# Performance work log

Hardware: AMD Instinct MI355X
Metric: run time of the kernel (lower is better)

The kernel has to match this reference:

```python
import jax, jax.numpy as jnp
import numpy as np

D_MODEL = 1024
N_HEADS = 16
HEAD_DIM = D_MODEL // N_HEADS


def setup_inputs() -> dict:
    key = jax.random.key(0)
    ks = jax.random.split(key, 9)
    B, S = 2, 2048
    s = 1.0 / np.sqrt(D_MODEL)
    return {
        "x": jax.random.normal(ks[0], (B, S, D_MODEL), dtype=jnp.float32),
        "Wq": jax.random.normal(ks[1], (D_MODEL, D_MODEL), dtype=jnp.float32) * s,
        "bq": jnp.zeros((D_MODEL,), dtype=jnp.float32),
        "Wk": jax.random.normal(ks[2], (D_MODEL, D_MODEL), dtype=jnp.float32) * s,
        "bk": jnp.zeros((D_MODEL,), dtype=jnp.float32),
        "Wv": jax.random.normal(ks[3], (D_MODEL, D_MODEL), dtype=jnp.float32) * s,
        "bv": jnp.zeros((D_MODEL,), dtype=jnp.float32),
        "Wo": jax.random.normal(ks[4], (D_MODEL, D_MODEL), dtype=jnp.float32) * s,
        "bo": jnp.zeros((D_MODEL,), dtype=jnp.float32),
    }


def reference(x, Wq, bq, Wk, bk, Wv, bv, Wo, bo):
    B, S, D = x.shape
    H, Hd = N_HEADS, HEAD_DIM
    # projections; torch Linear: x @ W^T + b -> here W stored as [in, out]
    q = (x @ Wq + bq).reshape(B, S, H, Hd).transpose(0, 2, 1, 3)  # [B,H,S,Hd]
    k = (x @ Wk + bk).reshape(B, S, H, Hd).transpose(0, 2, 1, 3)
    v = (x @ Wv + bv).reshape(B, S, H, Hd).transpose(0, 2, 1, 3)
    scores = jnp.einsum("bhsd,bhtd->bhst", q, k) / jnp.sqrt(jnp.float32(Hd))
    causal = jnp.tril(jnp.ones((S, S), dtype=bool))  # True = keep
    scores = jnp.where(causal, scores, jnp.float32(-jnp.inf))
    attn = jax.nn.softmax(scores, axis=-1)
    out = jnp.einsum("bhst,bhtd->bhsd", attn, v)  # [B,H,S,Hd]
    out = out.transpose(0, 2, 1, 3).reshape(B, S, D)
    return out @ Wo + bo
```

## Files before the change

### kernel.cpp

```cpp
#include <hip/hip_runtime.h>
#include <hip/hip_bf16.h>
#include <cmath>

#define D_MODEL 1024
#define N_HEADS 16
#define HEAD_DIM 64
#define SEQ 2048
#define BATCH 2
#define MROWS (BATCH * SEQ)

typedef __bf16 bf16;
typedef __bf16 bf16x8 __attribute__((ext_vector_type(8)));
typedef __bf16 bf16x4 __attribute__((ext_vector_type(4)));
typedef float f32x4 __attribute__((ext_vector_type(4)));

#define SWZG(row, cbyte) ((row) * 64 + ((cbyte) ^ ((((row) >> 1) & 3) << 4)))

#define GLOAD16(g, l)                                                        \
    __builtin_amdgcn_global_load_lds(                                        \
        (const __attribute__((address_space(1))) void*)(g),                  \
        (__attribute__((address_space(3))) void*)(l), 16, 0, 0)

static __device__ __forceinline__ unsigned short bfbits(float f) {
    bf16 b = (bf16)f;
    return *(unsigned short*)&b;
}

__global__ __launch_bounds__(256) void cvt_x(const float* __restrict__ x,
                                             bf16* __restrict__ xb) {
    int i = blockIdx.x * 256 + threadIdx.x;
    float4 v = ((const float4*)x)[i];
    bf16x4 o = { (bf16)v.x, (bf16)v.y, (bf16)v.z, (bf16)v.w };
    ((bf16x4*)xb)[i] = o;
}

__global__ void cvt_wt(const float* __restrict__ Wq, const float* __restrict__ Wk,
                       const float* __restrict__ Wv, const float* __restrict__ Wo,
                       bf16* __restrict__ wt) {
    __shared__ float tile[32][33];
    int z = blockIdx.z;
    const float* W = (z == 0) ? Wq : (z == 1) ? Wk : (z == 2) ? Wv : Wo;
    int n0 = blockIdx.x * 32, k0 = blockIdx.y * 32;
    int tx = threadIdx.x, ty = threadIdx.y;
    tile[ty][tx] = W[(size_t)(k0 + ty) * D_MODEL + n0 + tx];
    __syncthreads();
    wt[(size_t)z * D_MODEL * D_MODEL + (size_t)(n0 + ty) * D_MODEL + k0 + tx] =
        (bf16)tile[tx][ty];
}

template <int MODE>
__global__ __launch_bounds__(256) void gemm_k(const bf16* __restrict__ A,
                                              const bf16* __restrict__ Bt,
                                              const float* __restrict__ b0,
                                              const float* __restrict__ b1,
                                              const float* __restrict__ b2,
                                              void* __restrict__ outp) {
    constexpr int BM = 128, BK = 32, KDIM = D_MODEL;
    __shared__ alignas(16) char SMEM[49152];
    char* Asb = SMEM;
    char* Bsb = SMEM + 24576;
    const int tid = threadIdx.x;
    const int wid = tid >> 6, lane = tid & 63;
    const int m0 = blockIdx.y * BM, n0 = blockIdx.x * BM;
    const int wr = (wid >> 1) * 64, wc = (wid & 1) * 64;
    f32x4 acc[4][4] = {};

#define GSTAGE(K0, BUF)                                                       \
    {                                                                         \
        _Pragma("unroll") for (int c = 0; c < 2; ++c) {                       \
            const int q = c * 4 + wid;                                        \
            const int row = q * 16 + (lane >> 2);                             \
            const int col = (lane & 3) ^ ((row >> 1) & 3);                    \
            GLOAD16(&A[(size_t)(m0 + row) * KDIM + (K0) + col * 8],           \
                    Asb + (BUF) * 8192 + q * 1024);                           \
            GLOAD16(&Bt[(size_t)(n0 + row) * KDIM + (K0) + col * 8],          \
                    Bsb + (BUF) * 8192 + q * 1024);                           \
        }                                                                     \
    }

    GSTAGE(0, 0);
    GSTAGE(BK, 1);
    int cur = 0;
    for (int k0 = 0; k0 < KDIM; k0 += BK) {
        if (k0 + 2 * BK < KDIM) {
            int nb = cur + 2;
            if (nb >= 3) nb -= 3;
            GSTAGE(k0 + 2 * BK, nb);
            asm volatile("s_waitcnt vmcnt(8)" ::: "memory");
        } else if (k0 + BK < KDIM) {
            asm volatile("s_waitcnt vmcnt(4)" ::: "memory");
        } else {
            asm volatile("s_waitcnt vmcnt(0)" ::: "memory");
        }
        __builtin_amdgcn_s_barrier();

        char* Ab = Asb + cur * 8192;
        char* Bb = Bsb + cur * 8192;
        const int cb = (lane >> 4) * 16;
        bf16x8 a[4], b[4];
#pragma unroll
        for (int m = 0; m < 4; ++m) {
            int r = wr + m * 16 + (lane & 15);
            a[m] = *(bf16x8*)(Ab + SWZG(r, cb));
        }
#pragma unroll
        for (int n = 0; n < 4; ++n) {
            int r = wc + n * 16 + (lane & 15);
            b[n] = *(bf16x8*)(Bb + SWZG(r, cb));
        }
#pragma unroll
        for (int m = 0; m < 4; ++m)
#pragma unroll
            for (int n = 0; n < 4; ++n)
                acc[m][n] = __builtin_amdgcn_mfma_f32_16x16x32_bf16(a[m], b[n], acc[m][n], 0, 0, 0);

        __builtin_amdgcn_s_barrier();
        cur = (cur == 2) ? 0 : cur + 1;
    }
#undef GSTAGE

    const int z = n0 >> 10;
    const float* bias = (MODE == 1) ? b0 : ((z == 0) ? b0 : (z == 1) ? b1 : b2);

    if (MODE == 0 && z == 2) {
        bf16* T = (bf16*)SMEM;
#pragma unroll
        for (int m = 0; m < 4; ++m)
#pragma unroll
            for (int n = 0; n < 4; ++n)
#pragma unroll
                for (int r = 0; r < 4; ++r) {
                    int ml = wr + m * 16 + (lane >> 4) * 4 + r;
                    int nl = wc + n * 16 + (lane & 15);
                    float val = acc[m][n][r] + bias[(n0 & 1023) + nl];
                    *(bf16*)((char*)T + nl * 256 + ((2 * ml) ^ ((nl & 7) << 4))) = (bf16)val;
                }
        __builtin_amdgcn_s_barrier();
        const int b_ = m0 >> 11;
        const int s_base = m0 & 2047;
#pragma unroll
        for (int c = 0; c < 8; ++c) {
            int idx = c * 256 + tid;
            int nl = idx >> 4, j = idx & 15;
            bf16x8 v = *(bf16x8*)((char*)T + nl * 256 + ((16 * j) ^ ((nl & 7) << 4)));
            int colN = (n0 & 1023) + nl;
            int head = colN >> 6, hd = colN & 63;
            *(bf16x8*)&((bf16*)outp)[(size_t)2 * 4194304 +
                                     ((size_t)(b_ * N_HEADS + head) * HEAD_DIM + hd) * SEQ +
                                     s_base + 8 * j] = v;
        }
        return;
    }

#pragma unroll
    for (int m = 0; m < 4; ++m)
#pragma unroll
        for (int n = 0; n < 4; ++n)
#pragma unroll
            for (int r = 0; r < 4; ++r) {
                int grow = m0 + wr + m * 16 + (lane >> 4) * 4 + r;
                int gcol = n0 + wc + n * 16 + (lane & 15);
                if (MODE == 0) {
                    int colN = gcol & 1023;
                    float val = acc[m][n][r] + bias[colN];
                    if (z == 0) val *= 0.125f;
                    int b_ = grow >> 11, s_ = grow & 2047;
                    int h = colN >> 6, hd = colN & 63;
                    ((bf16*)outp)[(size_t)z * 4194304 +
                                  ((size_t)(b_ * N_HEADS + h) * SEQ + s_) * HEAD_DIM + hd] =
                        (bf16)val;
                } else {
                    float val = acc[m][n][r] + bias[gcol];
                    ((float*)outp)[(size_t)grow * D_MODEL + gcol] = val;
                }
            }
}

__global__ __launch_bounds__(512) void attn_k(const bf16* __restrict__ Qg,
                                              const bf16* __restrict__ Kg,
                                              const bf16* __restrict__ VTg,
                                              bf16* __restrict__ AO) {
    __shared__ alignas(16) bf16 Ks[2][64 * 64];
    __shared__ alignas(16) bf16 Vs[2][64 * 64];
    __shared__ alignas(16) unsigned int Pk[8][16][32];
    const int tid = threadIdx.x, wid = tid >> 6, lane = tid & 63;
    const int m = lane & 15, h = lane >> 4;
    const int band = 15 - (int)(blockIdx.x >> 5);
    const int bh = blockIdx.x & 31;
    const int q0 = band * 128 + wid * 16;
    const size_t base = (size_t)bh * SEQ * HEAD_DIM;
    const bf16* VT = VTg + (size_t)bh * HEAD_DIM * SEQ;
    const int swz = (m & 7) << 2;
    const int nt_w = band * 2 + (wid >> 2) + 1;
    const int nt_blk = band * 2 + 2;

    bf16x8 aq[2];
#pragma unroll
    for (int kc = 0; kc < 2; ++kc)
        aq[kc] = *(const bf16x8*)
            &Qg[base + (size_t)(q0 + m) * HEAD_DIM + kc * 32 + h * 8];

    f32x4 o[4] = {};
    float mrow = -__builtin_inff();
    float lrow = 0.f;

#define STAGE(T0, BUF)                                                            \
    {                                                                             \
        int row = tid >> 3, sl = tid & 7;                                         \
        GLOAD16(&Kg[base + (size_t)((T0) + row) * HEAD_DIM + 8 * (sl ^ (row & 7))], \
                (char*)&Ks[BUF][0] + tid * 16);                                   \
        GLOAD16(&VT[(size_t)row * SEQ + (T0) + 8 * (sl ^ (row & 7))],             \
                (char*)&Vs[BUF][0] + tid * 16);                                   \
    }

    STAGE(0, 0);
    int cur = 0;
    for (int it = 0; it < nt_blk; ++it) {
        if (it + 1 < nt_blk) {
            STAGE((it + 1) * 64, cur ^ 1);
            asm volatile("s_waitcnt vmcnt(2)" ::: "memory");
        } else {
            asm volatile("s_waitcnt vmcnt(0)" ::: "memory");
        }
        __builtin_amdgcn_s_barrier();

        if (it < nt_w) {
            const int t0 = it * 64;
            char* Kb = (char*)&Ks[cur][0];
            char* Vb = (char*)&Vs[cur][0];
            bf16x8 kf[4][2], vf[4][2];
#pragma unroll
            for (int tf = 0; tf < 4; ++tf)
#pragma unroll
                for (int kc = 0; kc < 2; ++kc)
                    kf[tf][kc] = *(bf16x8*)(Kb + (16 * tf + m) * 128 +
                                            (((4 * kc + h) ^ (m & 7)) << 4));
#pragma unroll
            for (int nf = 0; nf < 4; ++nf)
#pragma unroll
                for (int kc = 0; kc < 2; ++kc)
                    vf[nf][kc] = *(bf16x8*)(Vb + (16 * nf + m) * 128 +
                                            (((4 * kc + h) ^ (m & 7)) << 4));

            f32x4 s[4];
            __builtin_amdgcn_s_setprio(1);
#pragma unroll
            for (int tf = 0; tf < 4; ++tf) {
                f32x4 z = {};
                z = __builtin_amdgcn_mfma_f32_16x16x32_bf16(kf[tf][0], aq[0], z, 0, 0, 0);
                z = __builtin_amdgcn_mfma_f32_16x16x32_bf16(kf[tf][1], aq[1], z, 0, 0, 0);
                s[tf] = z;
            }
            __builtin_amdgcn_s_setprio(0);

            if (it == nt_w - 1) {
#pragma unroll
                for (int tf = 0; tf < 4; ++tf)
#pragma unroll
                    for (int r = 0; r < 4; ++r) {
                        int gq = q0 + m;
                        int gt = t0 + tf * 16 + h * 4 + r;
                        if (gt > gq) s[tf][r] = -__builtin_inff();
                    }
            }

            float mx = s[0][0];
#pragma unroll
            for (int tf = 0; tf < 4; ++tf)
#pragma unroll
                for (int r = 0; r < 4; ++r) mx = fmaxf(mx, s[tf][r]);
            mx = fmaxf(mx, __shfl_xor(mx, 16));
            mx = fmaxf(mx, __shfl_xor(mx, 32));
            if (!__all(mx <= mrow + 8.f)) {
                float mn = fmaxf(mrow, mx);
                float sf = __expf(mrow - mn);
                mrow = mn;
                lrow *= sf;
                float sfr[4];
#pragma unroll
                for (int r = 0; r < 4; ++r) sfr[r] = __shfl(sf, 20 * h + r);
#pragma unroll
                for (int nf = 0; nf < 4; ++nf)
#pragma unroll
                    for (int r = 0; r < 4; ++r) o[nf][r] *= sfr[r];
            }
            float rs = 0.f;
#pragma unroll
            for (int tf = 0; tf < 4; ++tf)
#pragma unroll
                for (int r = 0; r < 4; ++r) {
                    float pv = __expf(s[tf][r] - mrow);
                    s[tf][r] = pv;
                    rs += pv;
                }
            rs += __shfl_xor(rs, 16);
            rs += __shfl_xor(rs, 32);
            lrow += rs;

#pragma unroll
            for (int tf = 0; tf < 4; ++tf)
#pragma unroll
                for (int rp = 0; rp < 2; ++rp) {
                    unsigned int w = ((unsigned int)bfbits(s[tf][2 * rp + 1]) << 16) |
                                     bfbits(s[tf][2 * rp]);
                    Pk[wid][m][(8 * tf + 2 * h + rp) ^ swz] = w;
                }

            __builtin_amdgcn_s_setprio(1);
#pragma unroll
            for (int kc = 0; kc < 2; ++kc) {
                bf16x8 ap = *(bf16x8*)&Pk[wid][m][(16 * kc + 4 * h) ^ swz];
#pragma unroll
                for (int nf = 0; nf < 4; ++nf)
                    o[nf] = __builtin_amdgcn_mfma_f32_16x16x32_bf16(
                        ap, vf[nf][kc], o[nf], 0, 0, 0);
            }
            __builtin_amdgcn_s_setprio(0);
        }
        __builtin_amdgcn_s_barrier();
        cur ^= 1;
    }
#undef STAGE

    const int b_ = bh >> 4, hh = bh & 15;
    float lcr[4];
#pragma unroll
    for (int r = 0; r < 4; ++r) lcr[r] = __shfl(lrow, 20 * h + r);
#pragma unroll
    for (int nf = 0; nf < 4; ++nf)
#pragma unroll
        for (int r = 0; r < 4; ++r) {
            float val = o[nf][r] / lcr[r];
            int s_ = q0 + h * 4 + r;
            AO[((size_t)(b_ * SEQ + s_)) * D_MODEL + hh * HEAD_DIM + nf * 16 + m] =
                (bf16)val;
        }
}

extern "C" void kernel_launch(void* const* d_in, const int* in_sizes, int n_in,
                              void* d_out, int out_size, void* d_ws, size_t ws_size,
                              hipStream_t stream) {
    const float* x  = (const float*)d_in[0];
    const float* Wq = (const float*)d_in[1];
    const float* bq = (const float*)d_in[2];
    const float* Wk = (const float*)d_in[3];
    const float* bk = (const float*)d_in[4];
    const float* Wv = (const float*)d_in[5];
    const float* bv = (const float*)d_in[6];
    const float* Wo = (const float*)d_in[7];
    const float* bo = (const float*)d_in[8];

    char* ws = (char*)d_ws;
    const size_t MB = 1u << 20;
    bf16* wt = (bf16*)ws;
    bf16* xb = (bf16*)(ws + 8 * MB);
    bf16* Qb = (bf16*)(ws + 16 * MB);
    bf16* AO = (bf16*)(ws + 40 * MB);

    const size_t WSTRIDE = (size_t)D_MODEL * D_MODEL;

    cvt_x<<<dim3(MROWS * D_MODEL / 4 / 256), dim3(256), 0, stream>>>(x, xb);
    cvt_wt<<<dim3(32, 32, 4), dim3(32, 32), 0, stream>>>(Wq, Wk, Wv, Wo, wt);

    gemm_k<0><<<dim3(24, 32), dim3(256), 0, stream>>>(xb, wt, bq, bk, bv, Qb);

    bf16* Kb = Qb + 4194304;
    bf16* VTb = Qb + 2 * 4194304;
    attn_k<<<dim3(512), dim3(512), 0, stream>>>(Qb, Kb, VTb, AO);

    gemm_k<1><<<dim3(8, 32), dim3(256), 0, stream>>>(AO, wt + 3 * WSTRIDE, bo, bo, bo, d_out);
}
```

Before: 114.6 us.

## Split attention blocks into 64-row query tiles with interleaved causal ordering

The attention kernel moves from 512-thread blocks covering 128 query rows to 256-thread blocks covering 64 rows, and launches 1024 blocks. Block indices are mapped so heavy and light causal tiles alternate (descending from the top, then ascending), which balances load. Each thread now stages two K/V chunks per tile, with the wait count raised to match. The aim is to remove the idle waves that sat in the diagonal tile of the old 128-row blocks and to improve occupancy and tail balance, at the cost of loading K/V twice as often per query row.

```diff
diff --git a/kernel.cpp b/kernel.cpp
--- a/kernel.cpp
+++ b/kernel.cpp
@@ -176,23 +176,25 @@
             }
 }
 
-__global__ __launch_bounds__(512) void attn_k(const bf16* __restrict__ Qg,
+__global__ __launch_bounds__(256) void attn_k(const bf16* __restrict__ Qg,
                                               const bf16* __restrict__ Kg,
                                               const bf16* __restrict__ VTg,
                                               bf16* __restrict__ AO) {
     __shared__ alignas(16) bf16 Ks[2][64 * 64];
     __shared__ alignas(16) bf16 Vs[2][64 * 64];
-    __shared__ alignas(16) unsigned int Pk[8][16][32];
+    __shared__ alignas(16) unsigned int Pk[4][16][32];
     const int tid = threadIdx.x, wid = tid >> 6, lane = tid & 63;
     const int m = lane & 15, h = lane >> 4;
-    const int band = 15 - (int)(blockIdx.x >> 5);
-    const int bh = blockIdx.x & 31;
-    const int q0 = band * 128 + wid * 16;
+    const int idx = blockIdx.x;
+    const int bh = idx & 31;
+    const int a = (idx >> 5) & 7;
+    const int qd = idx >> 8;
+    const int hb = (qd == 0) ? (31 - a) : (qd == 1) ? (23 - a) : (qd == 2) ? (8 + a) : a;
+    const int q0 = hb * 64 + wid * 16;
     const size_t base = (size_t)bh * SEQ * HEAD_DIM;
     const bf16* VT = VTg + (size_t)bh * HEAD_DIM * SEQ;
     const int swz = (m & 7) << 2;
-    const int nt_w = band * 2 + (wid >> 2) + 1;
-    const int nt_blk = band * 2 + 2;
+    const int nt = hb + 1;
 
     bf16x8 aq[2];
 #pragma unroll
@@ -206,25 +208,29 @@
 
 #define STAGE(T0, BUF)                                                            \
     {                                                                             \
-        int row = tid >> 3, sl = tid & 7;                                         \
-        GLOAD16(&Kg[base + (size_t)((T0) + row) * HEAD_DIM + 8 * (sl ^ (row & 7))], \
-                (char*)&Ks[BUF][0] + tid * 16);                                   \
-        GLOAD16(&VT[(size_t)row * SEQ + (T0) + 8 * (sl ^ (row & 7))],             \
-                (char*)&Vs[BUF][0] + tid * 16);                                   \
+        _Pragma("unroll") for (int c = 0; c < 2; ++c) {                           \
+            int chunk = c * 256 + tid;                                            \
+            int row = chunk >> 3, sl = chunk & 7;                                 \
+            GLOAD16(&Kg[base + (size_t)((T0) + row) * HEAD_DIM +                  \
+                        8 * (sl ^ (row & 7))],                                    \
+                    (char*)&Ks[BUF][0] + chunk * 16);                             \
+            GLOAD16(&VT[(size_t)row * SEQ + (T0) + 8 * (sl ^ (row & 7))],         \
+                    (char*)&Vs[BUF][0] + chunk * 16);                             \
+        }                                                                         \
     }
 
     STAGE(0, 0);
     int cur = 0;
-    for (int it = 0; it < nt_blk; ++it) {
-        if (it + 1 < nt_blk) {
+    for (int it = 0; it < nt; ++it) {
+        if (it + 1 < nt) {
             STAGE((it + 1) * 64, cur ^ 1);
-            asm volatile("s_waitcnt vmcnt(2)" ::: "memory");
+            asm volatile("s_waitcnt vmcnt(4)" ::: "memory");
         } else {
             asm volatile("s_waitcnt vmcnt(0)" ::: "memory");
         }
         __builtin_amdgcn_s_barrier();
 
-        if (it < nt_w) {
+        {
             const int t0 = it * 64;
             char* Kb = (char*)&Ks[cur][0];
             char* Vb = (char*)&Vs[cur][0];
@@ -253,7 +259,7 @@
             }
             __builtin_amdgcn_s_setprio(0);
 
-            if (it == nt_w - 1) {
+            if (it == nt - 1) {
 #pragma unroll
                 for (int tf = 0; tf < 4; ++tf)
 #pragma unroll
@@ -366,7 +372,7 @@
 
     bf16* Kb = Qb + 4194304;
     bf16* VTb = Qb + 2 * 4194304;
-    attn_k<<<dim3(512), dim3(512), 0, stream>>>(Qb, Kb, VTb, AO);
+    attn_k<<<dim3(1024), dim3(256), 0, stream>>>(Qb, Kb, VTb, AO);
 
     gemm_k<1><<<dim3(8, 32), dim3(256), 0, stream>>>(AO, wt + 3 * WSTRIDE, bo, bo, bo, d_out);
 }
```

Result: faster. 111.3 us (-2.9%).
